# Performance work log

Measured on AMD Instinct MI355X. Metric: run time of the kernel, lower is better.

## Reference

```python
import jax, jax.numpy as jnp
import numpy as np

B, S, D = 8, 2048, 768
N_SPANS = 512
MAX_W = 30  # static max span width (inclusive width in tokens)
H = 100
NEG = -1e30


def setup_inputs() -> dict:
    key = jax.random.key(0)
    k1, k2, k3, k4, k5, k6 = jax.random.split(key, 6)
    seq_tensor = jax.random.normal(k1, (B, S, D), dtype=jnp.float32)
    starts = jax.random.randint(k2, (B, N_SPANS), 0, S - MAX_W)
    widths = jax.random.randint(k3, (B, N_SPANS), 1, MAX_W + 1)  # span length in [1, MAX_W]
    ends_excl = starts + widths  # exclusive end, as module expects
    span_indices = jnp.stack([starts, ends_excl], axis=-1).astype(jnp.int64)
    span_mask = (jax.random.uniform(k4, (B, N_SPANS)) > 0.1).astype(jnp.int32)
    att_w = jax.random.normal(k5, (D, 1), dtype=jnp.float32) / np.sqrt(D)
    att_b = jnp.zeros((1,), dtype=jnp.float32)
    ffnn_w = jax.random.normal(k6, (D, H), dtype=jnp.float32) / np.sqrt(D)
    ffnn_b = jnp.zeros((H,), dtype=jnp.float32)
    return {"seq_tensor": seq_tensor, "span_indices": span_indices, "span_mask": span_mask,
            "att_w": att_w, "att_b": att_b, "ffnn_w": ffnn_w, "ffnn_b": ffnn_b}


def reference(seq_tensor, span_indices, span_mask, att_w, att_b, ffnn_w, ffnn_b):
    # exclusive end -> inclusive end (span_end_is_exclusive=True)
    starts = span_indices[..., 0]
    ends = span_indices[..., 1] - 1
    widths = ends - starts  # inclusive width - 1, in [0, MAX_W-1]

    offsets = jnp.arange(MAX_W)  # [W]
    raw_idx = starts[..., None] + offsets  # [B, N, W]
    width_mask = offsets <= widths[..., None]  # [B, N, W]
    idx = jnp.where(width_mask, raw_idx, 0)

    # global attention logits over the sequence: [B, S]
    att_logits = (jnp.einsum('bsd,do->bso', seq_tensor, att_w) + att_b)[..., 0]

    # gather span token embeddings and logits: [B, N, W, D], [B, N, W]
    span_emb = jax.vmap(lambda seq, i: seq[i])(seq_tensor, idx)
    span_logits = jax.vmap(lambda lg, i: lg[i])(att_logits, idx)

    # masked softmax over span width
    span_logits = jnp.where(width_mask, span_logits, NEG)
    attn = jax.nn.softmax(span_logits, axis=-1)  # [B, N, W]

    attended = jnp.einsum('bnw,bnwd->bnd', attn, span_emb)  # [B, N, D]
    attended = attended * span_mask.astype(attended.dtype)[..., None]

    # FeedForward: 1 layer Linear + tanh (dropout=0)
    out = jnp.tanh(jnp.einsum('bnd,dh->bnh', attended, ffnn_w) + ffnn_b)
    return out
```

## Files before the change

### kernel.cpp

```cpp
#include <hip/hip_runtime.h>
#include <cstdint>
#include <cstddef>

#define NB 8
#define NS 2048
#define ND 768
#define NSP 512
#define MAXW 30
#define NH 100
#define LDP 104
#define NKS 24
#define NCF 8
#define ASTR 388

typedef __attribute__((ext_vector_type(8))) short short8;
typedef __attribute__((ext_vector_type(4))) float floatx4;

union U4S8 { uint4 v; short8 s8; unsigned u[4]; unsigned short us[8]; };

__device__ inline unsigned short f2bf(float f) {
    unsigned u = __float_as_uint(f);
    return (unsigned short)((u + 0x7fffu + ((u >> 16) & 1u)) >> 16);
}

__device__ inline void split2(float x0, float x1, unsigned& hi, unsigned& lo) {
    unsigned u0 = __float_as_uint(x0), u1 = __float_as_uint(x1);
    unsigned h0 = u0 & 0xFFFF0000u, h1 = u1 & 0xFFFF0000u;
    hi = (u0 >> 16) | h1;
    float r0 = x0 - __uint_as_float(h0);
    float r1 = x1 - __uint_as_float(h1);
    lo = (__float_as_uint(r0) >> 16) | (__float_as_uint(r1) & 0xFFFF0000u);
}

__global__ __launch_bounds__(256) void pack_b_kernel(
    const float* __restrict__ ffnn_w, const float* __restrict__ att_w,
    uint4* __restrict__ Bfrag)
{
    int ks = blockIdx.x;
    for (int idx = threadIdx.x; idx < NCF * 64; idx += 256) {
        int cf = idx >> 6, lane = idx & 63;
        int q = lane >> 4, r = lane & 15;
        int n = cf * 16 + r;
        U4S8 p;
#pragma unroll
        for (int j = 0; j < 8; j++) {
            int k = ks * 32 + q * 8 + j;
            float v = (n < NH) ? ffnn_w[(size_t)k * NH + n]
                               : (n == NH ? att_w[k] : 0.f);
            p.us[j] = f2bf(v);
        }
        Bfrag[(size_t)(ks * NCF + cf) * 64 + lane] = p.v;
    }
}

__global__ __launch_bounds__(256, 3) void proj_kernel(
    const float* __restrict__ seq, const uint4* __restrict__ Bfrag,
    float* __restrict__ P)
{
    __shared__ unsigned Ahi[16 * ASTR];
    __shared__ unsigned Alo[16 * ASTR];
    const int t = threadIdx.x;
    const int wave = t >> 6, lane = t & 63;
    const int q = lane >> 4, r = lane & 15;
    const int cf0 = wave * 2;
    const int row0 = blockIdx.x * 16;

    const int tr = t >> 4, tu = t & 15;
    const float4* gA = (const float4*)(seq + (size_t)(row0 + tr) * ND);
    float4 v[12];
#pragma unroll
    for (int j = 0; j < 12; ++j) v[j] = gA[tu + 16 * j];
#pragma unroll
    for (int j = 0; j < 12; ++j) {
        const int c = tu + 16 * j;
        unsigned h0, l0, h1, l1;
        split2(v[j].x, v[j].y, h0, l0);
        split2(v[j].z, v[j].w, h1, l1);
        uint2 uh; uh.x = h0; uh.y = h1;
        uint2 ul; ul.x = l0; ul.y = l1;
        *(uint2*)&Ahi[tr * ASTR + c * 2] = uh;
        *(uint2*)&Alo[tr * ASTR + c * 2] = ul;
    }
    __syncthreads();

    floatx4 acc[2] = {{0.f,0.f,0.f,0.f},{0.f,0.f,0.f,0.f}};
    const uint4* bp = Bfrag + (size_t)cf0 * 64 + lane;
    uint4 B0 = bp[0], B1 = bp[64];

    for (int ks = 0; ks < NKS; ++ks) {
        const int nk = (ks + 1 < NKS) ? ks + 1 : ks;
        uint4 N0 = bp[(size_t)nk * 512], N1 = bp[(size_t)nk * 512 + 64];
        U4S8 ah, al, b0, b1;
        ah.v = *(const uint4*)&Ahi[r * ASTR + ks * 16 + q * 4];
        al.v = *(const uint4*)&Alo[r * ASTR + ks * 16 + q * 4];
        b0.v = B0; b1.v = B1;
        acc[0] = __builtin_amdgcn_mfma_f32_16x16x32_bf16(ah.s8, b0.s8, acc[0], 0, 0, 0);
        acc[0] = __builtin_amdgcn_mfma_f32_16x16x32_bf16(al.s8, b0.s8, acc[0], 0, 0, 0);
        acc[1] = __builtin_amdgcn_mfma_f32_16x16x32_bf16(ah.s8, b1.s8, acc[1], 0, 0, 0);
        acc[1] = __builtin_amdgcn_mfma_f32_16x16x32_bf16(al.s8, b1.s8, acc[1], 0, 0, 0);
        B0 = N0; B1 = N1;
    }

#pragma unroll
    for (int c = 0; c < 2; ++c) {
        const int col = (cf0 + c) * 16 + r;
        if (col <= NH) {
#pragma unroll
            for (int reg = 0; reg < 4; ++reg)
                P[(size_t)(row0 + q * 4 + reg) * LDP + col] = acc[c][reg];
        }
    }
}

__global__ __launch_bounds__(256) void scan_kernel(
    const float* __restrict__ P, float* __restrict__ CS)
{
    __shared__ float4 sm[256];
    const int b = blockIdx.x / 26, chunk = blockIdx.x % 26;
    const int t = threadIdx.x;
    const size_t base = (size_t)b * NS;

    float4 v[8];
#pragma unroll
    for (int i = 0; i < 8; ++i) {
        const int s = t * 8 + i;
        const float* row = P + (base + s) * LDP;
        float el = __expf(row[100]);
        float4 x = *(const float4*)(row + chunk * 4);
        if (chunk == 25) { x.x = el; x.y = 0.f; x.z = 0.f; x.w = 0.f; }
        else { x.x *= el; x.y *= el; x.z *= el; x.w *= el; }
        v[i] = x;
    }
#pragma unroll
    for (int i = 1; i < 8; ++i) {
        v[i].x += v[i-1].x; v[i].y += v[i-1].y;
        v[i].z += v[i-1].z; v[i].w += v[i-1].w;
    }
    sm[t] = v[7];
    __syncthreads();
    for (int off = 1; off < 256; off <<= 1) {
        float4 add = {0.f,0.f,0.f,0.f};
        if (t >= off) add = sm[t - off];
        __syncthreads();
        if (t >= off) {
            float4 cur = sm[t];
            cur.x += add.x; cur.y += add.y; cur.z += add.z; cur.w += add.w;
            sm[t] = cur;
        }
        __syncthreads();
    }
    float4 pre = {0.f,0.f,0.f,0.f};
    if (t > 0) pre = sm[t - 1];
#pragma unroll
    for (int i = 0; i < 8; ++i) {
        float4 o = v[i];
        o.x += pre.x; o.y += pre.y; o.z += pre.z; o.w += pre.w;
        ((float4*)CS)[(base + t * 8 + i) * (LDP / 4) + chunk] = o;
    }
}

__global__ __launch_bounds__(256) void span_kernel(
    const int* __restrict__ span_idx, const int* __restrict__ span_mask,
    const float* __restrict__ CS, const float* __restrict__ ffnn_b,
    float* __restrict__ out)
{
    const int hw = threadIdx.x >> 5, lane = threadIdx.x & 31;
    const int gs = blockIdx.x * 8 + hw;
    const int b = gs / NSP;
    const int st = span_idx[2 * gs];
    int w = span_idx[2 * gs + 1] - st;
    w = max(1, min(w, MAXW));

    const int cl = min(lane, 25);
    const float4* cs4 = (const float4*)CS;
    const size_t rb = (size_t)b * NS;
    float4 hi = cs4[(rb + st + w - 1) * (LDP / 4) + cl];
    float4 lo = {0.f, 0.f, 0.f, 0.f};
    if (st > 0) lo = cs4[(rb + st - 1) * (LDP / 4) + cl];

    float4 d;
    d.x = hi.x - lo.x; d.y = hi.y - lo.y; d.z = hi.z - lo.z; d.w = hi.w - lo.w;
    float den = __shfl(d.x, 25, 32);
    float scale = (float)span_mask[gs] / den;

    if (lane < 25) {
        float4 bias = ((const float4*)ffnn_b)[lane];
        float4 o;
        o.x = tanhf(d.x * scale + bias.x);
        o.y = tanhf(d.y * scale + bias.y);
        o.z = tanhf(d.z * scale + bias.z);
        o.w = tanhf(d.w * scale + bias.w);
        *(float4*)(out + (size_t)gs * NH + 4 * lane) = o;
    }
}

extern "C" void kernel_launch(void* const* d_in, const int* in_sizes, int n_in,
                              void* d_out, int out_size, void* d_ws, size_t ws_size,
                              hipStream_t stream) {
    const float* seq      = (const float*)d_in[0];
    const int*   span_idx = (const int*)d_in[1];
    const int*   span_msk = (const int*)d_in[2];
    const float* att_w    = (const float*)d_in[3];
    const float* ffnn_w   = (const float*)d_in[5];
    const float* ffnn_b   = (const float*)d_in[6];
    float* out = (float*)d_out;

    char* ws = (char*)d_ws;
    size_t off = 0;
    float* P     = (float*)(ws + off); off += (size_t)NB * NS * LDP * 4;
    float* CS    = (float*)(ws + off); off += (size_t)NB * NS * LDP * 4;
    uint4* Bfrag = (uint4*)(ws + off);

    pack_b_kernel<<<NKS, 256, 0, stream>>>(ffnn_w, att_w, Bfrag);
    proj_kernel<<<(NB * NS) / 16, 256, 0, stream>>>(seq, Bfrag, P);
    scan_kernel<<<NB * (LDP / 4), 256, 0, stream>>>(P, CS);
    span_kernel<<<(NB * NSP) / 8, 256, 0, stream>>>(span_idx, span_msk, CS, ffnn_b, out);
}
```

Baseline: 122.4 us.

## Stream A tiles through small LDS buffer in proj; use wave-shuffle scan

The projection kernel no longer stages the whole 16x768 row block in shared memory. It loops over 12 K-chunks of 64, converting each chunk to hi/lo bf16 into a small LDS tile while prefetching the next chunk of seq and B fragments. This cuts LDS use so more blocks fit per CU (occupancy hint raised to 4). The cost is two barriers per iteration and less memory-level parallelism per block. The scan kernel also swaps its barrier-heavy shared-memory Hillis-Steele scan for an intra-wave shuffle scan plus a 4-entry cross-wave combine.

```diff
diff --git a/kernel.cpp b/kernel.cpp
--- a/kernel.cpp
+++ b/kernel.cpp
@@ -11,7 +11,8 @@
 #define LDP 104
 #define NKS 24
 #define NCF 8
-#define ASTR 388
+#define BM 16
+#define NIT 12
 
 typedef __attribute__((ext_vector_type(8))) short short8;
 typedef __attribute__((ext_vector_type(4))) float floatx4;
@@ -53,52 +54,54 @@
     }
 }
 
-__global__ __launch_bounds__(256, 3) void proj_kernel(
+__global__ __launch_bounds__(256, 4) void proj_kernel(
     const float* __restrict__ seq, const uint4* __restrict__ Bfrag,
     float* __restrict__ P)
 {
-    __shared__ unsigned Ahi[16 * ASTR];
-    __shared__ unsigned Alo[16 * ASTR];
+    __shared__ unsigned Ahi[BM][36];
+    __shared__ unsigned Alo[BM][36];
     const int t = threadIdx.x;
     const int wave = t >> 6, lane = t & 63;
     const int q = lane >> 4, r = lane & 15;
     const int cf0 = wave * 2;
-    const int row0 = blockIdx.x * 16;
-
-    const int tr = t >> 4, tu = t & 15;
-    const float4* gA = (const float4*)(seq + (size_t)(row0 + tr) * ND);
-    float4 v[12];
-#pragma unroll
-    for (int j = 0; j < 12; ++j) v[j] = gA[tu + 16 * j];
-#pragma unroll
-    for (int j = 0; j < 12; ++j) {
-        const int c = tu + 16 * j;
-        unsigned h0, l0, h1, l1;
-        split2(v[j].x, v[j].y, h0, l0);
-        split2(v[j].z, v[j].w, h1, l1);
-        uint2 uh; uh.x = h0; uh.y = h1;
-        uint2 ul; ul.x = l0; ul.y = l1;
-        *(uint2*)&Ahi[tr * ASTR + c * 2] = uh;
-        *(uint2*)&Alo[tr * ASTR + c * 2] = ul;
-    }
-    __syncthreads();
+    const int row0 = blockIdx.x * BM;
 
     floatx4 acc[2] = {{0.f,0.f,0.f,0.f},{0.f,0.f,0.f,0.f}};
+
+    const int sr = t >> 4, sc = t & 15;
+    const float4* gA = (const float4*)(seq + (size_t)(row0 + sr) * ND);
+    float4 sv = gA[sc];
+
     const uint4* bp = Bfrag + (size_t)cf0 * 64 + lane;
-    uint4 B0 = bp[0], B1 = bp[64];
-
-    for (int ks = 0; ks < NKS; ++ks) {
-        const int nk = (ks + 1 < NKS) ? ks + 1 : ks;
-        uint4 N0 = bp[(size_t)nk * 512], N1 = bp[(size_t)nk * 512 + 64];
-        U4S8 ah, al, b0, b1;
-        ah.v = *(const uint4*)&Ahi[r * ASTR + ks * 16 + q * 4];
-        al.v = *(const uint4*)&Alo[r * ASTR + ks * 16 + q * 4];
-        b0.v = B0; b1.v = B1;
-        acc[0] = __builtin_amdgcn_mfma_f32_16x16x32_bf16(ah.s8, b0.s8, acc[0], 0, 0, 0);
-        acc[0] = __builtin_amdgcn_mfma_f32_16x16x32_bf16(al.s8, b0.s8, acc[0], 0, 0, 0);
-        acc[1] = __builtin_amdgcn_mfma_f32_16x16x32_bf16(ah.s8, b1.s8, acc[1], 0, 0, 0);
-        acc[1] = __builtin_amdgcn_mfma_f32_16x16x32_bf16(al.s8, b1.s8, acc[1], 0, 0, 0);
-        B0 = N0; B1 = N1;
+    uint4 Bc0 = bp[0], Bc1 = bp[64], Bc2 = bp[512], Bc3 = bp[512 + 64];
+
+    for (int i = 0; i < NIT; ++i) {
+        unsigned h01, l01, h23, l23;
+        split2(sv.x, sv.y, h01, l01);
+        split2(sv.z, sv.w, h23, l23);
+        __syncthreads();
+        { uint2 u; u.x = h01; u.y = h23; *(uint2*)&Ahi[sr][sc * 2] = u; }
+        { uint2 u; u.x = l01; u.y = l23; *(uint2*)&Alo[sr][sc * 2] = u; }
+        __syncthreads();
+
+        const int ni = (i + 1 < NIT) ? i + 1 : i;
+        sv = gA[ni * 16 + sc];
+        const size_t nb = (size_t)ni * 1024;
+        uint4 Bn0 = bp[nb], Bn1 = bp[nb + 64], Bn2 = bp[nb + 512], Bn3 = bp[nb + 512 + 64];
+
+#pragma unroll
+        for (int ksl = 0; ksl < 2; ++ksl) {
+            U4S8 ah, al, b0, b1;
+            ah.v = *(const uint4*)&Ahi[r][ksl * 16 + q * 4];
+            al.v = *(const uint4*)&Alo[r][ksl * 16 + q * 4];
+            b0.v = ksl ? Bc2 : Bc0;
+            b1.v = ksl ? Bc3 : Bc1;
+            acc[0] = __builtin_amdgcn_mfma_f32_16x16x32_bf16(ah.s8, b0.s8, acc[0], 0, 0, 0);
+            acc[0] = __builtin_amdgcn_mfma_f32_16x16x32_bf16(al.s8, b0.s8, acc[0], 0, 0, 0);
+            acc[1] = __builtin_amdgcn_mfma_f32_16x16x32_bf16(ah.s8, b1.s8, acc[1], 0, 0, 0);
+            acc[1] = __builtin_amdgcn_mfma_f32_16x16x32_bf16(al.s8, b1.s8, acc[1], 0, 0, 0);
+        }
+        Bc0 = Bn0; Bc1 = Bn1; Bc2 = Bn2; Bc3 = Bn3;
     }
 
 #pragma unroll
@@ -115,9 +118,10 @@
 __global__ __launch_bounds__(256) void scan_kernel(
     const float* __restrict__ P, float* __restrict__ CS)
 {
-    __shared__ float4 sm[256];
-    const int b = blockIdx.x / 26, chunk = blockIdx.x % 26;
-    const int t = threadIdx.x;
+    __shared__ float4 smw[4];
+    const int bidx = blockIdx.x;
+    const int b = bidx / 26, chunk = bidx - b * 26;
+    const int t = threadIdx.x, lane = t & 63, wv = t >> 6;
     const size_t base = (size_t)b * NS;
 
     float4 v[8];
@@ -136,25 +140,38 @@
         v[i].x += v[i-1].x; v[i].y += v[i-1].y;
         v[i].z += v[i-1].z; v[i].w += v[i-1].w;
     }
-    sm[t] = v[7];
+
+    float4 tot = v[7];
+#pragma unroll
+    for (int off = 1; off < 64; off <<= 1) {
+        float4 n;
+        n.x = __shfl_up(tot.x, off); n.y = __shfl_up(tot.y, off);
+        n.z = __shfl_up(tot.z, off); n.w = __shfl_up(tot.w, off);
+        if (lane >= off) {
+            tot.x += n.x; tot.y += n.y; tot.z += n.z; tot.w += n.w;
+        }
+    }
+    float4 ex;
+    ex.x = __shfl_up(tot.x, 1); ex.y = __shfl_up(tot.y, 1);
+    ex.z = __shfl_up(tot.z, 1); ex.w = __shfl_up(tot.w, 1);
+    if (lane == 0) { ex.x = 0.f; ex.y = 0.f; ex.z = 0.f; ex.w = 0.f; }
+
+    if (lane == 63) smw[wv] = tot;
     __syncthreads();
-    for (int off = 1; off < 256; off <<= 1) {
-        float4 add = {0.f,0.f,0.f,0.f};
-        if (t >= off) add = sm[t - off];
-        __syncthreads();
-        if (t >= off) {
-            float4 cur = sm[t];
-            cur.x += add.x; cur.y += add.y; cur.z += add.z; cur.w += add.w;
-            sm[t] = cur;
-        }
-        __syncthreads();
-    }
-    float4 pre = {0.f,0.f,0.f,0.f};
-    if (t > 0) pre = sm[t - 1];
+    float4 woff = {0.f, 0.f, 0.f, 0.f};
+#pragma unroll
+    for (int j = 0; j < 4; ++j) {
+        if (j < wv) {
+            float4 s = smw[j];
+            woff.x += s.x; woff.y += s.y; woff.z += s.z; woff.w += s.w;
+        }
+    }
+    ex.x += woff.x; ex.y += woff.y; ex.z += woff.z; ex.w += woff.w;
+
 #pragma unroll
     for (int i = 0; i < 8; ++i) {
         float4 o = v[i];
-        o.x += pre.x; o.y += pre.y; o.z += pre.z; o.w += pre.w;
+        o.x += ex.x; o.y += ex.y; o.z += ex.z; o.w += ex.w;
         ((float4*)CS)[(base + t * 8 + i) * (LDP / 4) + chunk] = o;
     }
 }
@@ -212,7 +229,7 @@
     uint4* Bfrag = (uint4*)(ws + off);
 
     pack_b_kernel<<<NKS, 256, 0, stream>>>(ffnn_w, att_w, Bfrag);
-    proj_kernel<<<(NB * NS) / 16, 256, 0, stream>>>(seq, Bfrag, P);
+    proj_kernel<<<(NB * NS) / BM, 256, 0, stream>>>(seq, Bfrag, P);
     scan_kernel<<<NB * (LDP / 4), 256, 0, stream>>>(P, CS);
     span_kernel<<<(NB * NSP) / 8, 256, 0, stream>>>(span_idx, span_msk, CS, ffnn_b, out);
 }
```

Result: faster. 117.0 us (-4.4%).
